# Optimization experiments

Measured on AMD Instinct MI355X. Metric: run time of the kernel, lower is better.

The kernel has to match this reference:

```python
import jax, jax.numpy as jnp
import numpy as np

PAD_IDX = 0
K = 5
TEMPERATURE = 1.0
BATCH = 256
VOCAB = 50257


def setup_inputs() -> dict:
    key = jax.random.key(0)
    k1, k2, k3, k4, k5 = jax.random.split(key, 5)
    draft_tokens = jax.random.randint(k1, (BATCH, K), 0, VOCAB)
    # valid-ish log-probabilities (negative values)
    draft_log_probs = -jax.random.uniform(k2, (BATCH, K), minval=0.05, maxval=8.0, dtype=jnp.float32)
    target_logits = jax.random.normal(k3, (BATCH, K, VOCAB), dtype=jnp.float32)
    random_vals = jax.random.uniform(k4, (BATCH, K), dtype=jnp.float32)
    uniform_sample = jax.random.uniform(k5, (BATCH,), dtype=jnp.float32)
    return {
        "draft_tokens": draft_tokens,
        "draft_log_probs": draft_log_probs,
        "target_logits": target_logits,
        "random_vals": random_vals,
        "uniform_sample": uniform_sample,
    }


def reference(draft_tokens, draft_log_probs, target_logits, random_vals, uniform_sample):
    B, k = draft_tokens.shape
    # --- accept/reject scan ---
    tlp = jax.nn.log_softmax(target_logits / TEMPERATURE, axis=-1)          # [B,k,V]
    tlp_draft = jnp.take_along_axis(tlp, draft_tokens[..., None], axis=2)[..., 0]  # [B,k]
    accept_probs = jnp.minimum(jnp.exp(tlp_draft - draft_log_probs), 1.0)
    accepted_mask = random_vals < accept_probs
    rejected_sent = jnp.concatenate(
        [~accepted_mask, jnp.ones((B, 1), dtype=bool)], axis=1)              # [B,k+1]
    first_reject = jnp.argmax(rejected_sent, axis=1)                         # [B]
    n_accepted = first_reject
    # fixed-width (k) accepted_tokens, PAD-filled past n_accepted (jit-friendly
    # variant of torch's dynamic max_accepted truncation; same valid entries)
    pos = jnp.arange(k)[None, :]
    accepted_tokens = jnp.where(pos < n_accepted[:, None], draft_tokens, PAD_IDX)
    # --- vectorized fallback sampling at first reject position ---
    rp = jnp.minimum(first_reject, k - 1)                                    # clamp for gather
    sel_logits = jnp.take_along_axis(target_logits, rp[:, None, None], axis=1)[:, 0, :]  # [B,V]
    target_probs = jax.nn.softmax(sel_logits / TEMPERATURE, axis=-1)
    dlp_sel = jnp.take_along_axis(draft_log_probs, rp[:, None], axis=1)      # [B,1]
    # torch builds a constant vector exp(dlp) over the whole vocab
    draft_probs = jnp.exp(dlp_sel)                                           # [B,1] broadcasts
    adjusted = jnp.clip(target_probs - draft_probs, 0.0)
    s = adjusted.sum(axis=-1, keepdims=True)
    probs = jnp.where(s > 0, adjusted / jnp.where(s > 0, s, 1.0), target_probs)  # [B,V]
    # multinomial(probs, 1) via inverse CDF with provided uniform sample
    cdf = jnp.cumsum(probs, axis=-1)
    thresh = uniform_sample[:, None] * cdf[:, -1:]
    sampled = jnp.argmax(cdf >= thresh, axis=-1)                             # [B]
    final_tokens = jnp.where(first_reject < k, sampled, PAD_IDX)
    return accepted_tokens, n_accepted, final_tokens
```

## Files before the change

kernel.cpp:

```cpp
#include <hip/hip_runtime.h>
#include <math.h>
#include <stdint.h>

#define VOCAB 50257
#define KD 5
#define NBATCH 256
#define NT 1024
#define NW (NT / 64)
#define TILE 1024
#define NTILES ((VOCAB + TILE - 1) / TILE)

__global__ __launch_bounds__(NT) void spec_decode_kernel(
    const int* __restrict__ dtok,
    const float* __restrict__ dlp,
    const float* __restrict__ logits,
    const float* __restrict__ rnd,
    const float* __restrict__ usmp,
    int* __restrict__ out)
{
    const int b    = blockIdx.x;
    const int tid  = threadIdx.x;
    const int lane = tid & 63;
    const int wv   = tid >> 6;

    __shared__ double s_w[NW];
    __shared__ double s_tileA[NTILES];
    __shared__ double s_tileR[NTILES];
    __shared__ double s_dbc[2];
    __shared__ int    s_ibc[2];
    __shared__ int    s_c[NW];

    double Zsel  = 0.0;
    int    n_acc = KD;
    for (int r = 0; r < KD; ++r) {
        const float* row = logits + ((size_t)b * KD + r) * (size_t)VOCAB;
        const int head = (int)((4u - ((((uintptr_t)row) >> 2) & 3u)) & 3u);

        float tlogit = 0.f, dl = 0.f, rv = 0.f;
        if (tid == 0) {
            int tok = dtok[b * KD + r];
            tlogit  = row[tok];
            dl      = dlp[b * KD + r];
            rv      = rnd[b * KD + r];
        }

        double l0 = 0.0, l1 = 0.0;
        if (tid < head) l0 += (double)expf(row[tid]);
        const int nvec = (VOCAB - head) >> 2;
        const float4* row4 = (const float4*)(row + head);
        for (int i = tid; i < nvec; i += NT) {
            float4 x = row4[i];
            l0 += (double)expf(x.x) + (double)expf(x.y);
            l1 += (double)expf(x.z) + (double)expf(x.w);
        }
        const int tail_start = head + (nvec << 2);
        const int tail_cnt   = VOCAB - tail_start;
        if (tid < tail_cnt) l1 += (double)expf(row[tail_start + tid]);

        double local = l0 + l1;
        for (int off = 32; off; off >>= 1) local += __shfl_down(local, off, 64);
        if (lane == 0) s_w[wv] = local;
        __syncthreads();
        if (wv == 0) {
            double v = (lane < NW) ? s_w[lane] : 0.0;
            for (int off = 8; off; off >>= 1) v += __shfl_down(v, off, 64);
            if (lane == 0) {
                double Z   = v;
                double tlp = (double)tlogit - log(Z);
                double ap  = exp(tlp - (double)dl);
                if (ap > 1.0) ap = 1.0;
                s_dbc[0] = Z;
                s_ibc[0] = ((double)rv < ap) ? 1 : 0;
            }
        }
        __syncthreads();
        Zsel = s_dbc[0];
        int acc = s_ibc[0];
        if (!acc) { n_acc = r; break; }
    }

    if (tid == 0) {
        for (int r = 0; r < KD; ++r)
            out[b * KD + r] = (r < n_acc) ? dtok[b * KD + r] : 0;
        out[NBATCH * KD + b] = n_acc;
        if (n_acc >= KD) out[NBATCH * KD + NBATCH + b] = 0;
    }
    if (n_acc >= KD) return;

    const int    rp   = n_acc;
    const float* row  = logits + ((size_t)b * KD + rp) * (size_t)VOCAB;
    const double invZ = 1.0 / Zsel;
    const double dp   = exp((double)dlp[b * KD + rp]);
    const int    head = (int)((4u - ((((uintptr_t)row) >> 2) & 3u)) & 3u);

    for (int t = wv; t < NTILES; t += NW) {
        const int start = t * TILE;
        int end = start + TILE; if (end > VOCAB) end = VOCAB;
        double aS = 0.0, rS = 0.0;
        if (lane < head) {
            double p = exp((double)row[start + lane]) * invZ;
            rS += p;
            double a = p - dp;
            if (a > 0.0) aS += a;
        }
        const int vcnt = (end - start - head) >> 2;
        const float4* v4 = (const float4*)(row + start + head);
        for (int j = lane; j < vcnt; j += 64) {
            float4 x = v4[j];
            double p0 = exp((double)x.x) * invZ;
            double p1 = exp((double)x.y) * invZ;
            double p2 = exp((double)x.z) * invZ;
            double p3 = exp((double)x.w) * invZ;
            rS += p0 + p1 + p2 + p3;
            double a0 = p0 - dp; if (a0 > 0.0) aS += a0;
            double a1 = p1 - dp; if (a1 > 0.0) aS += a1;
            double a2 = p2 - dp; if (a2 > 0.0) aS += a2;
            double a3 = p3 - dp; if (a3 > 0.0) aS += a3;
        }
        const int ts = start + head + (vcnt << 2);
        if (lane < end - ts) {
            double p = exp((double)row[ts + lane]) * invZ;
            rS += p;
            double a = p - dp;
            if (a > 0.0) aS += a;
        }
        for (int off = 32; off; off >>= 1) {
            aS += __shfl_down(aS, off, 64);
            rS += __shfl_down(rS, off, 64);
        }
        if (lane == 0) { s_tileA[t] = aS; s_tileR[t] = rS; }
    }
    __syncthreads();

    if (wv == 0) {
        double a  = (lane < NTILES) ? s_tileA[lane] : 0.0;
        double rr = (lane < NTILES) ? s_tileR[lane] : 0.0;
        double sa = a, sr = rr;
        for (int off = 1; off < 64; off <<= 1) {
            double va = __shfl_up(sa, (unsigned)off, 64); if (lane >= off) sa += va;
            double vr = __shfl_up(sr, (unsigned)off, 64); if (lane >= off) sr += vr;
        }
        double S      = __shfl(sa, NTILES - 1, 64);
        int    useAdj = (S > 0.0) ? 1 : 0;
        double Tot    = useAdj ? S : __shfl(sr, NTILES - 1, 64);
        double T      = (double)usmp[b] * Tot;
        double incl   = useAdj ? sa : sr;
        double tval   = useAdj ? a : rr;
        bool crossed  = (lane < NTILES) && (incl >= T);
        unsigned long long mk = __ballot(crossed);
        int ct = mk ? (int)(__ffsll(mk) - 1) : (NTILES - 1);
        double P = __shfl(incl, ct, 64) - __shfl(tval, ct, 64);
        if (lane == 0) {
            s_dbc[0] = P;
            s_dbc[1] = T;
            s_ibc[0] = ct;
            s_ibc[1] = useAdj;
        }
    }
    __syncthreads();

    {
        double Pb     = s_dbc[0];
        double T      = s_dbc[1];
        int    ct     = s_ibc[0];
        int    useAdj = s_ibc[1];
        int    idx    = ct * TILE + tid;
        double g      = 0.0;
        if (idx < VOCAB) {
            double p = exp((double)row[idx]) * invZ;
            if (useAdj) {
                double a = p - dp;
                g = (a > 0.0) ? a : 0.0;
            } else {
                g = p;
            }
        }
        double sc = g;
        for (int off = 1; off < 64; off <<= 1) {
            double v = __shfl_up(sc, (unsigned)off, 64);
            if (lane >= off) sc += v;
        }
        if (lane == 63) s_w[wv] = sc;
        __syncthreads();
        double woff = 0.0;
        for (int w = 0; w < wv; ++w) woff += s_w[w];
        double incl = Pb + woff + sc;
        bool cross = (idx < VOCAB) && (incl >= T);
        unsigned long long mk = __ballot(cross);
        if (lane == 0)
            s_c[wv] = mk ? (int)(wv * 64 + __ffsll(mk) - 1) : 0x7FFFFFFF;
        __syncthreads();
        if (tid == 0) {
            int best = 0x7FFFFFFF;
            for (int w = 0; w < NW; ++w) best = min(best, s_c[w]);
            int smp;
            if (best == 0x7FFFFFFF) {
                smp = ct * TILE + TILE - 1;
                if (smp > VOCAB - 1) smp = VOCAB - 1;
            } else {
                smp = ct * TILE + best;
            }
            out[NBATCH * KD + NBATCH + b] = smp;
        }
    }
}

extern "C" void kernel_launch(void* const* d_in, const int* in_sizes, int n_in,
                              void* d_out, int out_size, void* d_ws, size_t ws_size,
                              hipStream_t stream) {
    const int*   dtok   = (const int*)d_in[0];
    const float* dlp    = (const float*)d_in[1];
    const float* logits = (const float*)d_in[2];
    const float* rnd    = (const float*)d_in[3];
    const float* usmp   = (const float*)d_in[4];
    int*         out    = (int*)d_out;
    (void)in_sizes; (void)n_in; (void)out_size; (void)d_ws; (void)ws_size;
    spec_decode_kernel<<<dim3(NBATCH), dim3(NT), 0, stream>>>(
        dtok, dlp, logits, rnd, usmp, out);
}
```

Baseline: 332.0 us.

## Keep exp values in registers from the softmax pass to reuse in sampling

The log-sum-exp pass now stores each thread's fp32 exp values in a 13x4 register array, plus head and tail elements in shared memory. The fallback sampling pass reuses these instead of rereading the rejected row from global memory and recomputing double-precision exp. The tile layout changes from 1024-element contiguous tiles to per-thread slots that are reduced across waves. This removes a second full read of the row and the fp64 exp work, at the cost of 52 extra registers per thread at a 1024-thread block size. It also changes the rounding of probabilities, since exp is now fp32 rather than fp64.

```diff
diff --git a/kernel.cpp b/kernel.cpp
--- a/kernel.cpp
+++ b/kernel.cpp
@@ -7,8 +7,8 @@
 #define NBATCH 256
 #define NT 1024
 #define NW (NT / 64)
-#define TILE 1024
-#define NTILES ((VOCAB + TILE - 1) / TILE)
+#define NSLOT 13
+#define NSEG (NSLOT + 2)
 
 __global__ __launch_bounds__(NT) void spec_decode_kernel(
     const int* __restrict__ dtok,
@@ -24,17 +24,25 @@
     const int wv   = tid >> 6;
 
     __shared__ double s_w[NW];
-    __shared__ double s_tileA[NTILES];
-    __shared__ double s_tileR[NTILES];
-    __shared__ double s_dbc[2];
-    __shared__ int    s_ibc[2];
+    __shared__ double s_pA[NSLOT][NW + 1];
+    __shared__ double s_pR[NSLOT][NW + 1];
+    __shared__ double s_ht[6];
+    __shared__ double s_db[2];
+    __shared__ int    s_ib[2];
     __shared__ int    s_c[NW];
 
-    double Zsel  = 0.0;
-    int    n_acc = KD;
+    float ef[NSLOT][4];
+
+    double       Zsel  = 0.0;
+    int          n_acc = KD;
+    int          headS = 0, nvecS = 0;
+    const float* rowS  = nullptr;
+
     for (int r = 0; r < KD; ++r) {
         const float* row = logits + ((size_t)b * KD + r) * (size_t)VOCAB;
-        const int head = (int)((4u - ((((uintptr_t)row) >> 2) & 3u)) & 3u);
+        const int  head = (int)((4u - ((((uintptr_t)row) >> 2) & 3u)) & 3u);
+        const int  nvec = (VOCAB - head) >> 2;
+        const float4* row4 = (const float4*)(row + head);
 
         float tlogit = 0.f, dl = 0.f, rv = 0.f;
         if (tid == 0) {
@@ -45,17 +53,37 @@
         }
 
         double l0 = 0.0, l1 = 0.0;
-        if (tid < head) l0 += (double)expf(row[tid]);
-        const int nvec = (VOCAB - head) >> 2;
-        const float4* row4 = (const float4*)(row + head);
-        for (int i = tid; i < nvec; i += NT) {
-            float4 x = row4[i];
-            l0 += (double)expf(x.x) + (double)expf(x.y);
-            l1 += (double)expf(x.z) + (double)expf(x.w);
+        if (tid < head) {
+            double eh = (double)expf(row[tid]);
+            l0 += eh;
+            s_ht[tid] = eh;
+        }
+        #pragma unroll
+        for (int c = 0; c < NSLOT - 1; ++c) {
+            float4 x = row4[c * NT + tid];
+            float e0 = expf(x.x), e1 = expf(x.y), e2 = expf(x.z), e3 = expf(x.w);
+            ef[c][0] = e0; ef[c][1] = e1; ef[c][2] = e2; ef[c][3] = e3;
+            l0 += (double)e0 + (double)e1;
+            l1 += (double)e2 + (double)e3;
+        }
+        {
+            int i = (NSLOT - 1) * NT + tid;
+            if (i < nvec) {
+                float4 x = row4[i];
+                float e0 = expf(x.x), e1 = expf(x.y), e2 = expf(x.z), e3 = expf(x.w);
+                ef[NSLOT - 1][0] = e0; ef[NSLOT - 1][1] = e1;
+                ef[NSLOT - 1][2] = e2; ef[NSLOT - 1][3] = e3;
+                l0 += (double)e0 + (double)e1;
+                l1 += (double)e2 + (double)e3;
+            }
         }
         const int tail_start = head + (nvec << 2);
         const int tail_cnt   = VOCAB - tail_start;
-        if (tid < tail_cnt) l1 += (double)expf(row[tail_start + tid]);
+        if (tid < tail_cnt) {
+            double et = (double)expf(row[tail_start + tid]);
+            l1 += et;
+            s_ht[3 + tid] = et;
+        }
 
         double local = l0 + l1;
         for (int off = 32; off; off >>= 1) local += __shfl_down(local, off, 64);
@@ -69,13 +97,14 @@
                 double tlp = (double)tlogit - log(Z);
                 double ap  = exp(tlp - (double)dl);
                 if (ap > 1.0) ap = 1.0;
-                s_dbc[0] = Z;
-                s_ibc[0] = ((double)rv < ap) ? 1 : 0;
-            }
-        }
-        __syncthreads();
-        Zsel = s_dbc[0];
-        int acc = s_ibc[0];
+                s_db[0] = Z;
+                s_ib[0] = ((double)rv < ap) ? 1 : 0;
+            }
+        }
+        __syncthreads();
+        Zsel  = s_db[0];
+        int acc = s_ib[0];
+        headS = head; nvecS = nvec; rowS = row;
         if (!acc) { n_acc = r; break; }
     }
 
@@ -87,95 +116,98 @@
     }
     if (n_acc >= KD) return;
 
-    const int    rp   = n_acc;
-    const float* row  = logits + ((size_t)b * KD + rp) * (size_t)VOCAB;
     const double invZ = 1.0 / Zsel;
-    const double dp   = exp((double)dlp[b * KD + rp]);
-    const int    head = (int)((4u - ((((uintptr_t)row) >> 2) & 3u)) & 3u);
-
-    for (int t = wv; t < NTILES; t += NW) {
-        const int start = t * TILE;
-        int end = start + TILE; if (end > VOCAB) end = VOCAB;
+    const double dp   = exp((double)dlp[b * KD + n_acc]);
+    const int    head = headS;
+    const int    nvec = nvecS;
+    const float4* row4 = (const float4*)(rowS + head);
+
+    #pragma unroll
+    for (int c = 0; c < NSLOT; ++c) {
         double aS = 0.0, rS = 0.0;
-        if (lane < head) {
-            double p = exp((double)row[start + lane]) * invZ;
-            rS += p;
-            double a = p - dp;
-            if (a > 0.0) aS += a;
-        }
-        const int vcnt = (end - start - head) >> 2;
-        const float4* v4 = (const float4*)(row + start + head);
-        for (int j = lane; j < vcnt; j += 64) {
-            float4 x = v4[j];
-            double p0 = exp((double)x.x) * invZ;
-            double p1 = exp((double)x.y) * invZ;
-            double p2 = exp((double)x.z) * invZ;
-            double p3 = exp((double)x.w) * invZ;
-            rS += p0 + p1 + p2 + p3;
-            double a0 = p0 - dp; if (a0 > 0.0) aS += a0;
-            double a1 = p1 - dp; if (a1 > 0.0) aS += a1;
-            double a2 = p2 - dp; if (a2 > 0.0) aS += a2;
-            double a3 = p3 - dp; if (a3 > 0.0) aS += a3;
-        }
-        const int ts = start + head + (vcnt << 2);
-        if (lane < end - ts) {
-            double p = exp((double)row[ts + lane]) * invZ;
-            rS += p;
-            double a = p - dp;
-            if (a > 0.0) aS += a;
+        bool v = (c < NSLOT - 1) || ((NSLOT - 1) * NT + tid < nvec);
+        if (v) {
+            #pragma unroll
+            for (int e = 0; e < 4; ++e) {
+                double p = (double)ef[c][e] * invZ;
+                rS += p;
+                double a = p - dp;
+                if (a > 0.0) aS += a;
+            }
         }
         for (int off = 32; off; off >>= 1) {
             aS += __shfl_down(aS, off, 64);
             rS += __shfl_down(rS, off, 64);
         }
-        if (lane == 0) { s_tileA[t] = aS; s_tileR[t] = rS; }
+        if (lane == 0) { s_pA[c][wv] = aS; s_pR[c][wv] = rS; }
     }
     __syncthreads();
 
     if (wv == 0) {
-        double a  = (lane < NTILES) ? s_tileA[lane] : 0.0;
-        double rr = (lane < NTILES) ? s_tileR[lane] : 0.0;
-        double sa = a, sr = rr;
-        for (int off = 1; off < 64; off <<= 1) {
+        double A = 0.0, R = 0.0;
+        if (lane >= 1 && lane <= NSLOT) {
+            #pragma unroll
+            for (int w = 0; w < NW; ++w) { A += s_pA[lane - 1][w]; R += s_pR[lane - 1][w]; }
+        } else if (lane == 0) {
+            for (int j = 0; j < head; ++j) {
+                double p = s_ht[j] * invZ;
+                R += p;
+                double a = p - dp; if (a > 0.0) A += a;
+            }
+        } else if (lane == NSEG - 1) {
+            int tcnt = VOCAB - head - (nvec << 2);
+            for (int j = 0; j < tcnt; ++j) {
+                double p = s_ht[3 + j] * invZ;
+                R += p;
+                double a = p - dp; if (a > 0.0) A += a;
+            }
+        }
+        double sa = A, sr = R;
+        for (int off = 1; off < 16; off <<= 1) {
             double va = __shfl_up(sa, (unsigned)off, 64); if (lane >= off) sa += va;
             double vr = __shfl_up(sr, (unsigned)off, 64); if (lane >= off) sr += vr;
         }
-        double S      = __shfl(sa, NTILES - 1, 64);
-        int    useAdj = (S > 0.0) ? 1 : 0;
-        double Tot    = useAdj ? S : __shfl(sr, NTILES - 1, 64);
+        double SA     = __shfl(sa, NSEG - 1, 64);
+        int    useAdj = (SA > 0.0) ? 1 : 0;
+        double Tot    = useAdj ? SA : __shfl(sr, NSEG - 1, 64);
         double T      = (double)usmp[b] * Tot;
         double incl   = useAdj ? sa : sr;
-        double tval   = useAdj ? a : rr;
-        bool crossed  = (lane < NTILES) && (incl >= T);
+        double val    = useAdj ? A  : R;
+        bool crossed  = (lane < NSEG) && (incl >= T);
         unsigned long long mk = __ballot(crossed);
-        int ct = mk ? (int)(__ffsll(mk) - 1) : (NTILES - 1);
-        double P = __shfl(incl, ct, 64) - __shfl(tval, ct, 64);
+        int    cseg = mk ? (int)(__ffsll(mk) - 1) : (NSEG - 1);
+        double Pex  = __shfl(incl, cseg, 64) - __shfl(val, cseg, 64);
         if (lane == 0) {
-            s_dbc[0] = P;
-            s_dbc[1] = T;
-            s_ibc[0] = ct;
-            s_ibc[1] = useAdj;
+            s_db[0] = Pex; s_db[1] = T;
+            s_ib[0] = cseg; s_ib[1] = useAdj;
         }
     }
     __syncthreads();
 
-    {
-        double Pb     = s_dbc[0];
-        double T      = s_dbc[1];
-        int    ct     = s_ibc[0];
-        int    useAdj = s_ibc[1];
-        int    idx    = ct * TILE + tid;
-        double g      = 0.0;
-        if (idx < VOCAB) {
-            double p = exp((double)row[idx]) * invZ;
-            if (useAdj) {
-                double a = p - dp;
-                g = (a > 0.0) ? a : 0.0;
-            } else {
-                g = p;
-            }
-        }
-        double sc = g;
+    const double P      = s_db[0];
+    const double T      = s_db[1];
+    const int    cseg   = s_ib[0];
+    const int    useAdj = s_ib[1];
+
+    if (cseg >= 1 && cseg <= NSLOT) {
+        const int  c     = cseg - 1;
+        const int  i4    = c * NT + tid;
+        const bool valid = i4 < nvec;
+        double c0 = 0, c1 = 0, c2 = 0, c3 = 0, tsum = 0;
+        if (valid) {
+            float4 x = row4[i4];
+            double p0 = (double)expf(x.x) * invZ;
+            double p1 = (double)expf(x.y) * invZ;
+            double p2 = (double)expf(x.z) * invZ;
+            double p3 = (double)expf(x.w) * invZ;
+            double g0 = useAdj ? fmax(p0 - dp, 0.0) : p0;
+            double g1 = useAdj ? fmax(p1 - dp, 0.0) : p1;
+            double g2 = useAdj ? fmax(p2 - dp, 0.0) : p2;
+            double g3 = useAdj ? fmax(p3 - dp, 0.0) : p3;
+            c0 = g0; c1 = c0 + g1; c2 = c1 + g2; c3 = c2 + g3;
+            tsum = c3;
+        }
+        double sc = tsum;
         for (int off = 1; off < 64; off <<= 1) {
             double v = __shfl_up(sc, (unsigned)off, 64);
             if (lane >= off) sc += v;
@@ -184,24 +216,56 @@
         __syncthreads();
         double woff = 0.0;
         for (int w = 0; w < wv; ++w) woff += s_w[w];
-        double incl = Pb + woff + sc;
-        bool cross = (idx < VOCAB) && (incl >= T);
-        unsigned long long mk = __ballot(cross);
+        double base = P + woff + (sc - tsum);
+        int bj = -1;
+        if (valid) {
+            if      (base + c0 >= T) bj = 0;
+            else if (base + c1 >= T) bj = 1;
+            else if (base + c2 >= T) bj = 2;
+            else if (base + c3 >= T) bj = 3;
+        }
+        unsigned long long mk = __ballot(bj >= 0);
+        int L  = mk ? (int)(__ffsll(mk) - 1) : 0;
+        int jl = __shfl(bj, L, 64);
         if (lane == 0)
-            s_c[wv] = mk ? (int)(wv * 64 + __ffsll(mk) - 1) : 0x7FFFFFFF;
+            s_c[wv] = mk ? (head + 4 * (c * NT + wv * 64 + L) + jl) : 0x7FFFFFFF;
         __syncthreads();
         if (tid == 0) {
             int best = 0x7FFFFFFF;
             for (int w = 0; w < NW; ++w) best = min(best, s_c[w]);
             int smp;
             if (best == 0x7FFFFFFF) {
-                smp = ct * TILE + TILE - 1;
-                if (smp > VOCAB - 1) smp = VOCAB - 1;
+                int endv = c * NT + NT; if (endv > nvec) endv = nvec;
+                smp = head + 4 * endv - 1;
             } else {
-                smp = ct * TILE + best;
+                smp = best;
             }
             out[NBATCH * KD + NBATCH + b] = smp;
         }
+    } else if (tid == 0) {
+        int smp = -1;
+        if (cseg == 0) {
+            double cum = P;
+            for (int j = 0; j < head; ++j) {
+                double p = s_ht[j] * invZ;
+                double g = useAdj ? fmax(p - dp, 0.0) : p;
+                cum += g;
+                if (cum >= T) { smp = j; break; }
+            }
+            if (smp < 0) smp = (head > 0) ? head - 1 : 0;
+        } else {
+            int ts   = head + (nvec << 2);
+            int tcnt = VOCAB - ts;
+            double cum = P;
+            for (int j = 0; j < tcnt; ++j) {
+                double p = s_ht[3 + j] * invZ;
+                double g = useAdj ? fmax(p - dp, 0.0) : p;
+                cum += g;
+                if (cum >= T) { smp = ts + j; break; }
+            }
+            if (smp < 0) smp = VOCAB - 1;
+        }
+        out[NBATCH * KD + NBATCH + b] = smp;
     }
 }
 
```

New measurement: 340.5 us. +2.6%, slower.
